# Kernel optimization log

Hardware: AMD Instinct MI355X
Metric: run time of the kernel (lower is better)

Reference implementation:

```python
import jax, jax.numpy as jnp
import numpy as np

B, N = 8192, 4096
OUT_DIM = 32


def setup_inputs() -> dict:
    key = jax.random.key(0)
    k_rr, k_drop, k_w1, k_b1, k_w2, k_b2 = jax.random.split(key, 6)
    rr = jax.random.uniform(k_rr, (B, N), dtype=jnp.float32, minval=0.4, maxval=1.4)
    drop = jax.random.uniform(k_drop, (B, N)) < 0.3
    rr = jnp.where(drop, 0.0, rr)
    # projection MLP params (Linear(6,16) -> ReLU -> Dropout(eval: identity) -> Linear(16,32))
    w1 = jax.random.normal(k_w1, (6, 16), dtype=jnp.float32) * (1.0 / np.sqrt(6))
    b1 = jax.random.normal(k_b1, (16,), dtype=jnp.float32) * 0.01
    w2 = jax.random.normal(k_w2, (16, OUT_DIM), dtype=jnp.float32) * (1.0 / np.sqrt(16))
    b2 = jax.random.normal(k_b2, (OUT_DIM,), dtype=jnp.float32) * 0.01
    return {"rr_intervals": rr, "w1": w1, "b1": b1, "w2": w2, "b2": b2}


def _hrv_features(rr):
    # rr: (B, N) float32, zero-padded. Faithful to the per-row torch loop, vectorized.
    dt = rr.dtype
    mask = rr > 0                                   # (B, N)
    cnt = jnp.sum(mask, axis=1)                     # (B,) int
    cntf = cnt.astype(dt)
    # masked mean / unbiased std (torch.std default ddof=1)
    denom_m = jnp.maximum(cntf, 1.0)
    mean_rr = jnp.sum(jnp.where(mask, rr, 0.0), axis=1) / denom_m
    dev = jnp.where(mask, rr - mean_rr[:, None], 0.0)
    var = jnp.sum(dev * dev, axis=1) / jnp.maximum(cntf - 1.0, 1.0)
    sdnn = jnp.sqrt(var)
    # compact valid entries to the front (stable -> preserves order), so diffs
    # match torch.diff(rr[rr > 0])
    order = jnp.argsort(jnp.logical_not(mask), axis=1, stable=True)  # (B, N)
    compact = jnp.take_along_axis(rr, order, axis=1)                  # (B, N)
    diffs = compact[:, 1:] - compact[:, :-1]                          # (B, N-1)
    dmask = jnp.arange(N - 1)[None, :] < (cnt - 1)[:, None]           # valid diffs
    ndiff = jnp.maximum(cntf - 1.0, 1.0)
    rmssd = jnp.sqrt(jnp.sum(jnp.where(dmask, diffs * diffs, 0.0), axis=1) / ndiff)
    nn50 = jnp.sum(((jnp.abs(diffs) > 0.05) & dmask).astype(dt), axis=1)
    pnn50 = nn50 / ndiff
    hr = 60.0 / jnp.maximum(mean_rr, 1e-12)
    cv = sdnn / jnp.maximum(mean_rr, 1e-12)
    feats = jnp.stack([mean_rr, sdnn, rmssd, pnn50, hr, cv], axis=1)  # (B, 6)
    feats = jnp.where((cnt > 1)[:, None], feats, 0.0)
    # per-column batch normalization, applied only where column max > 0
    col_max = jnp.max(feats, axis=0)
    col_mean = jnp.mean(feats, axis=0)
    col_std = jnp.std(feats, axis=0, ddof=1)
    normed = (feats - col_mean[None, :]) / (col_std[None, :] + 1e-8)
    feats = jnp.where((col_max > 0)[None, :], normed, feats)
    return feats


def reference(rr_intervals, w1, b1, w2, b2):
    feats = _hrv_features(rr_intervals)                 # (B, 6)
    h = jax.nn.relu(feats @ w1 + b1)                    # (B, 16); dropout in eval = identity
    return h @ w2 + b2                                  # (B, OUT_DIM)
```

## Files before the change

### kernel.cpp

```cpp
#include <hip/hip_runtime.h>
#include <math.h>

#define BATCH 8192
#define NLEN 4096
#define THREADS 256
#define PER_THREAD (NLEN / THREADS)

__global__ __launch_bounds__(THREADS) void hrv_feats_kernel(
    const float* __restrict__ rr, float* __restrict__ feats) {
    __shared__ float sh_last[THREADS];
    __shared__ unsigned char sh_has[THREADS];
    __shared__ double sh_sum[4], sh_sumsq[4], sh_sumd2[4];
    __shared__ int sh_cnt[4], sh_nn50[4];

    const int row = ((blockIdx.x & 7) << 10) | (blockIdx.x >> 3);
    const int t = threadIdx.x;
    const float* r = rr + (size_t)row * NLEN + t * PER_THREAD;

    float x[PER_THREAD];
    float4* xv = reinterpret_cast<float4*>(x);
    const float4* rv = reinterpret_cast<const float4*>(r);
#pragma unroll
    for (int i = 0; i < PER_THREAD / 4; ++i) xv[i] = rv[i];

    float sum = 0.f, sumsq = 0.f, sumd2 = 0.f;
    int cnt = 0, nn50 = 0;
    float first = 0.f, last = 0.f;
    int has = 0;
#pragma unroll
    for (int i = 0; i < PER_THREAD; ++i) {
        float v = x[i];
        if (v > 0.f) {
            sum += v;
            sumsq += v * v;
            ++cnt;
            if (has) {
                float d = v - last;
                sumd2 += d * d;
                nn50 += (fabsf(d) > 0.05f) ? 1 : 0;
            } else {
                first = v;
                has = 1;
            }
            last = v;
        }
    }
    sh_last[t] = last;
    sh_has[t] = (unsigned char)has;
    __syncthreads();
    if (has && t > 0) {
        for (int j = t - 1; j >= 0; --j) {
            if (sh_has[j]) {
                float d = first - sh_last[j];
                sumd2 += d * d;
                nn50 += (fabsf(d) > 0.05f) ? 1 : 0;
                break;
            }
        }
    }

    double dsum = sum, dsumsq = sumsq, dsumd2 = sumd2;
    int icnt = cnt, inn = nn50;
#pragma unroll
    for (int off = 32; off > 0; off >>= 1) {
        dsum += __shfl_down(dsum, off, 64);
        dsumsq += __shfl_down(dsumsq, off, 64);
        dsumd2 += __shfl_down(dsumd2, off, 64);
        icnt += __shfl_down(icnt, off, 64);
        inn += __shfl_down(inn, off, 64);
    }
    const int wave = t >> 6;
    if ((t & 63) == 0) {
        sh_sum[wave] = dsum;
        sh_sumsq[wave] = dsumsq;
        sh_sumd2[wave] = dsumd2;
        sh_cnt[wave] = icnt;
        sh_nn50[wave] = inn;
    }
    __syncthreads();
    if (t == 0) {
        double S = 0, S2 = 0, D2 = 0;
        int C = 0, NN = 0;
        for (int w = 0; w < 4; ++w) {
            S += sh_sum[w];
            S2 += sh_sumsq[w];
            D2 += sh_sumd2[w];
            C += sh_cnt[w];
            NN += sh_nn50[w];
        }
        const float cntf = (float)C;
        const float denom_m = fmaxf(cntf, 1.f);
        const float mean = (float)(S / (double)denom_m);
        const float varsum = (float)(S2 - (double)C * (double)mean * (double)mean);
        const float denom_v = fmaxf(cntf - 1.f, 1.f);
        const float sdnn = sqrtf(fmaxf(varsum / denom_v, 0.f));
        const float rmssd = sqrtf(fmaxf((float)(D2 / (double)denom_v), 0.f));
        const float pnn50 = (float)NN / denom_v;
        const float hr = 60.f / fmaxf(mean, 1e-12f);
        const float cv = sdnn / fmaxf(mean, 1e-12f);
        float f[6] = {mean, sdnn, rmssd, pnn50, hr, cv};
        if (C <= 1) {
#pragma unroll
            for (int c = 0; c < 6; ++c) f[c] = 0.f;
        }
#pragma unroll
        for (int c = 0; c < 6; ++c) feats[c * BATCH + row] = f[c];
    }
}

__global__ __launch_bounds__(256) void stats_mlp_kernel(
    const float* __restrict__ feats,
    const float* __restrict__ w1, const float* __restrict__ b1,
    const float* __restrict__ w2, const float* __restrict__ b2,
    float* __restrict__ out) {
    __shared__ float sh_w[656];
    __shared__ double sh_s[4][6], sh_s2[4][6];
    __shared__ float sh_m[4][6];
    __shared__ float sh_stats[18];

    const int t = threadIdx.x;

    for (int i = t; i < 656; i += 256) {
        float v;
        if (i < 96) v = w1[i];
        else if (i < 112) v = b1[i - 96];
        else if (i < 624) v = w2[i - 112];
        else v = b2[i - 624];
        sh_w[i] = v;
    }

    double s[6], s2[6];
    float mx[6];
#pragma unroll
    for (int c = 0; c < 6; ++c) { s[c] = 0.0; s2[c] = 0.0; mx[c] = -INFINITY; }

#pragma unroll
    for (int cp = 0; cp < 3; ++cp) {
        const float4* c0 =
            reinterpret_cast<const float4*>(feats + (2 * cp) * BATCH);
        const float4* c1 =
            reinterpret_cast<const float4*>(feats + (2 * cp + 1) * BATCH);
        float4 buf[16];
#pragma unroll
        for (int k = 0; k < 8; ++k) buf[k] = c0[t + k * 256];
#pragma unroll
        for (int k = 0; k < 8; ++k) buf[8 + k] = c1[t + k * 256];
#pragma unroll
        for (int k = 0; k < 16; ++k) {
            const int c = 2 * cp + (k >> 3);
            const float f[4] = {buf[k].x, buf[k].y, buf[k].z, buf[k].w};
#pragma unroll
            for (int e = 0; e < 4; ++e) {
                s[c] += (double)f[e];
                s2[c] += (double)f[e] * (double)f[e];
                mx[c] = fmaxf(mx[c], f[e]);
            }
        }
    }
#pragma unroll
    for (int off = 32; off; off >>= 1) {
#pragma unroll
        for (int c = 0; c < 6; ++c) {
            s[c] += __shfl_down(s[c], off, 64);
            s2[c] += __shfl_down(s2[c], off, 64);
            mx[c] = fmaxf(mx[c], __shfl_down(mx[c], off, 64));
        }
    }
    if ((t & 63) == 0) {
        const int w = t >> 6;
#pragma unroll
        for (int c = 0; c < 6; ++c) {
            sh_s[w][c] = s[c];
            sh_s2[w][c] = s2[c];
            sh_m[w][c] = mx[c];
        }
    }
    __syncthreads();
    if (t < 6) {
        double S = 0, S2 = 0;
        float M = -INFINITY;
        for (int w = 0; w < 4; ++w) {
            S += sh_s[w][t];
            S2 += sh_s2[w][t];
            M = fmaxf(M, sh_m[w][t]);
        }
        const double meanb = S / (double)BATCH;
        double var = (S2 - (double)BATCH * meanb * meanb) / (double)(BATCH - 1);
        if (var < 0.0) var = 0.0;
        sh_stats[t] = (float)meanb;
        sh_stats[6 + t] = (float)sqrt(var);
        sh_stats[12 + t] = M;
    }
    __syncthreads();

    const int row = blockIdx.x * 256 + t;
    float f[6];
#pragma unroll
    for (int c = 0; c < 6; ++c) {
        float v = feats[c * BATCH + row];
        if (sh_stats[12 + c] > 0.f)
            v = (v - sh_stats[c]) / (sh_stats[6 + c] + 1e-8f);
        f[c] = v;
    }
    float h[16];
#pragma unroll
    for (int j = 0; j < 16; ++j) {
        float a = sh_w[96 + j];
#pragma unroll
        for (int c = 0; c < 6; ++c) a = fmaf(f[c], sh_w[c * 16 + j], a);
        h[j] = fmaxf(a, 0.f);
    }
    float o[32];
#pragma unroll
    for (int k = 0; k < 32; ++k) o[k] = sh_w[624 + k];
#pragma unroll
    for (int j = 0; j < 16; ++j) {
        const float hj = h[j];
#pragma unroll
        for (int k = 0; k < 32; ++k) o[k] = fmaf(hj, sh_w[112 + j * 32 + k], o[k]);
    }
    float4* ov = reinterpret_cast<float4*>(out + (size_t)row * 32);
    const float4* op = reinterpret_cast<const float4*>(o);
#pragma unroll
    for (int i = 0; i < 8; ++i) ov[i] = op[i];
}

extern "C" void kernel_launch(void* const* d_in, const int* in_sizes, int n_in,
                              void* d_out, int out_size, void* d_ws, size_t ws_size,
                              hipStream_t stream) {
    const float* rr = (const float*)d_in[0];
    const float* w1 = (const float*)d_in[1];
    const float* b1 = (const float*)d_in[2];
    const float* w2 = (const float*)d_in[3];
    const float* b2 = (const float*)d_in[4];
    float* out = (float*)d_out;
    float* feats = (float*)d_ws;

    hrv_feats_kernel<<<BATCH, THREADS, 0, stream>>>(rr, feats);
    stats_mlp_kernel<<<BATCH / 256, THREADS, 0, stream>>>(feats, w1, b1, w2, b2, out);
}
```

Baseline: 39.22 us.

## Process four rows per block with register double-buffered prefetch of the next row

Each block of the feature kernel now handles four consecutive rows instead of one. The next row's data is loaded into a second register buffer while the current row is reduced, and the shared scratch arrays are double-buffered by row parity. The aim is to hide global load latency behind the reduction and cut per-block launch and teardown overhead. In exchange, register pressure doubles for the row buffer and the grid shrinks to 2048 blocks, which can reduce occupancy and memory-level parallelism.

New measurement: 47.79 us. +21.8%, slower.

```diff
diff --git a/kernel.cpp b/kernel.cpp
--- a/kernel.cpp
+++ b/kernel.cpp
@@ -5,106 +5,126 @@
 #define NLEN 4096
 #define THREADS 256
 #define PER_THREAD (NLEN / THREADS)
+#define RPB 4
+#define NBLK (BATCH / RPB)
 
 __global__ __launch_bounds__(THREADS) void hrv_feats_kernel(
     const float* __restrict__ rr, float* __restrict__ feats) {
-    __shared__ float sh_last[THREADS];
-    __shared__ unsigned char sh_has[THREADS];
-    __shared__ double sh_sum[4], sh_sumsq[4], sh_sumd2[4];
-    __shared__ int sh_cnt[4], sh_nn50[4];
-
-    const int row = ((blockIdx.x & 7) << 10) | (blockIdx.x >> 3);
+    __shared__ float sh_last[2][THREADS];
+    __shared__ unsigned char sh_has[2][THREADS];
+    __shared__ double sh_sum[2][4], sh_sumsq[2][4], sh_sumd2[2][4];
+    __shared__ int sh_cnt[2][4], sh_nn50[2][4];
+
     const int t = threadIdx.x;
-    const float* r = rr + (size_t)row * NLEN + t * PER_THREAD;
-
-    float x[PER_THREAD];
-    float4* xv = reinterpret_cast<float4*>(x);
-    const float4* rv = reinterpret_cast<const float4*>(r);
-#pragma unroll
-    for (int i = 0; i < PER_THREAD / 4; ++i) xv[i] = rv[i];
-
-    float sum = 0.f, sumsq = 0.f, sumd2 = 0.f;
-    int cnt = 0, nn50 = 0;
-    float first = 0.f, last = 0.f;
-    int has = 0;
-#pragma unroll
-    for (int i = 0; i < PER_THREAD; ++i) {
-        float v = x[i];
-        if (v > 0.f) {
-            sum += v;
-            sumsq += v * v;
-            ++cnt;
-            if (has) {
-                float d = v - last;
-                sumd2 += d * d;
-                nn50 += (fabsf(d) > 0.05f) ? 1 : 0;
-            } else {
-                first = v;
-                has = 1;
-            }
-            last = v;
-        }
-    }
-    sh_last[t] = last;
-    sh_has[t] = (unsigned char)has;
-    __syncthreads();
-    if (has && t > 0) {
-        for (int j = t - 1; j >= 0; --j) {
-            if (sh_has[j]) {
-                float d = first - sh_last[j];
-                sumd2 += d * d;
-                nn50 += (fabsf(d) > 0.05f) ? 1 : 0;
-                break;
-            }
-        }
-    }
-
-    double dsum = sum, dsumsq = sumsq, dsumd2 = sumd2;
-    int icnt = cnt, inn = nn50;
-#pragma unroll
-    for (int off = 32; off > 0; off >>= 1) {
-        dsum += __shfl_down(dsum, off, 64);
-        dsumsq += __shfl_down(dsumsq, off, 64);
-        dsumd2 += __shfl_down(dsumd2, off, 64);
-        icnt += __shfl_down(icnt, off, 64);
-        inn += __shfl_down(inn, off, 64);
-    }
-    const int wave = t >> 6;
-    if ((t & 63) == 0) {
-        sh_sum[wave] = dsum;
-        sh_sumsq[wave] = dsumsq;
-        sh_sumd2[wave] = dsumd2;
-        sh_cnt[wave] = icnt;
-        sh_nn50[wave] = inn;
-    }
-    __syncthreads();
-    if (t == 0) {
-        double S = 0, S2 = 0, D2 = 0;
-        int C = 0, NN = 0;
-        for (int w = 0; w < 4; ++w) {
-            S += sh_sum[w];
-            S2 += sh_sumsq[w];
-            D2 += sh_sumd2[w];
-            C += sh_cnt[w];
-            NN += sh_nn50[w];
-        }
-        const float cntf = (float)C;
-        const float denom_m = fmaxf(cntf, 1.f);
-        const float mean = (float)(S / (double)denom_m);
-        const float varsum = (float)(S2 - (double)C * (double)mean * (double)mean);
-        const float denom_v = fmaxf(cntf - 1.f, 1.f);
-        const float sdnn = sqrtf(fmaxf(varsum / denom_v, 0.f));
-        const float rmssd = sqrtf(fmaxf((float)(D2 / (double)denom_v), 0.f));
-        const float pnn50 = (float)NN / denom_v;
-        const float hr = 60.f / fmaxf(mean, 1e-12f);
-        const float cv = sdnn / fmaxf(mean, 1e-12f);
-        float f[6] = {mean, sdnn, rmssd, pnn50, hr, cv};
-        if (C <= 1) {
-#pragma unroll
-            for (int c = 0; c < 6; ++c) f[c] = 0.f;
-        }
-#pragma unroll
-        for (int c = 0; c < 6; ++c) feats[c * BATCH + row] = f[c];
+    const int chunk = ((blockIdx.x & 7) << 8) | (blockIdx.x >> 3);
+    const int row0 = chunk * RPB;
+    const float* base = rr + (size_t)row0 * NLEN + t * PER_THREAD;
+
+    float x[2][PER_THREAD];
+    {
+        const float4* rv = reinterpret_cast<const float4*>(base);
+        float4* xv = reinterpret_cast<float4*>(x[0]);
+#pragma unroll
+        for (int i = 0; i < PER_THREAD / 4; ++i) xv[i] = rv[i];
+    }
+
+#pragma unroll
+    for (int r = 0; r < RPB; ++r) {
+        const int pb = r & 1;
+        if (r < RPB - 1) {
+            const float4* rv =
+                reinterpret_cast<const float4*>(base + (size_t)(r + 1) * NLEN);
+            float4* xv = reinterpret_cast<float4*>(x[pb ^ 1]);
+#pragma unroll
+            for (int i = 0; i < PER_THREAD / 4; ++i) xv[i] = rv[i];
+        }
+
+        float sum = 0.f, sumsq = 0.f, sumd2 = 0.f;
+        int cnt = 0, nn50 = 0;
+        float first = 0.f, last = 0.f;
+        int has = 0;
+#pragma unroll
+        for (int i = 0; i < PER_THREAD; ++i) {
+            float v = x[pb][i];
+            if (v > 0.f) {
+                sum += v;
+                sumsq += v * v;
+                ++cnt;
+                if (has) {
+                    float d = v - last;
+                    sumd2 += d * d;
+                    nn50 += (fabsf(d) > 0.05f) ? 1 : 0;
+                } else {
+                    first = v;
+                    has = 1;
+                }
+                last = v;
+            }
+        }
+        sh_last[pb][t] = last;
+        sh_has[pb][t] = (unsigned char)has;
+        __syncthreads();
+        if (has && t > 0) {
+            for (int j = t - 1; j >= 0; --j) {
+                if (sh_has[pb][j]) {
+                    float d = first - sh_last[pb][j];
+                    sumd2 += d * d;
+                    nn50 += (fabsf(d) > 0.05f) ? 1 : 0;
+                    break;
+                }
+            }
+        }
+
+        double dsum = sum, dsumsq = sumsq, dsumd2 = sumd2;
+        int icnt = cnt, inn = nn50;
+#pragma unroll
+        for (int off = 32; off > 0; off >>= 1) {
+            dsum += __shfl_down(dsum, off, 64);
+            dsumsq += __shfl_down(dsumsq, off, 64);
+            dsumd2 += __shfl_down(dsumd2, off, 64);
+            icnt += __shfl_down(icnt, off, 64);
+            inn += __shfl_down(inn, off, 64);
+        }
+        const int wave = t >> 6;
+        if ((t & 63) == 0) {
+            sh_sum[pb][wave] = dsum;
+            sh_sumsq[pb][wave] = dsumsq;
+            sh_sumd2[pb][wave] = dsumd2;
+            sh_cnt[pb][wave] = icnt;
+            sh_nn50[pb][wave] = inn;
+        }
+        __syncthreads();
+        if (t == 0) {
+            double S = 0, S2 = 0, D2 = 0;
+            int C = 0, NN = 0;
+#pragma unroll
+            for (int w = 0; w < 4; ++w) {
+                S += sh_sum[pb][w];
+                S2 += sh_sumsq[pb][w];
+                D2 += sh_sumd2[pb][w];
+                C += sh_cnt[pb][w];
+                NN += sh_nn50[pb][w];
+            }
+            const float cntf = (float)C;
+            const float denom_m = fmaxf(cntf, 1.f);
+            const float mean = (float)(S / (double)denom_m);
+            const float varsum =
+                (float)(S2 - (double)C * (double)mean * (double)mean);
+            const float denom_v = fmaxf(cntf - 1.f, 1.f);
+            const float sdnn = sqrtf(fmaxf(varsum / denom_v, 0.f));
+            const float rmssd = sqrtf(fmaxf((float)(D2 / (double)denom_v), 0.f));
+            const float pnn50 = (float)NN / denom_v;
+            const float hr = 60.f / fmaxf(mean, 1e-12f);
+            const float cv = sdnn / fmaxf(mean, 1e-12f);
+            float f[6] = {mean, sdnn, rmssd, pnn50, hr, cv};
+            if (C <= 1) {
+#pragma unroll
+                for (int c = 0; c < 6; ++c) f[c] = 0.f;
+            }
+            const int row = row0 + r;
+#pragma unroll
+            for (int c = 0; c < 6; ++c) feats[c * BATCH + row] = f[c];
+        }
     }
 }
 
@@ -236,6 +256,6 @@
     float* out = (float*)d_out;
     float* feats = (float*)d_ws;
 
-    hrv_feats_kernel<<<BATCH, THREADS, 0, stream>>>(rr, feats);
+    hrv_feats_kernel<<<NBLK, THREADS, 0, stream>>>(rr, feats);
     stats_mlp_kernel<<<BATCH / 256, THREADS, 0, stream>>>(feats, w1, b1, w2, b2, out);
 }
```
